# Kernel optimization log

Measured on AMD Instinct MI355X. Metric: run time of the kernel, lower is better.

## Reference

```python
import jax, jax.numpy as jnp
import numpy as np

N, F, E = 50000, 128, 800000
H, C1, C2 = 4, 32, 32  # heads, channel_in, channel_out
LRELU_SLOPE = 0.2
LN_EPS = 1e-5


def _gat_conv(x, src, dst, W_src, W_dst, att_src, att_dst, bias, n, h, c):
    # x: [n, f_in]; src/dst: [e] edge endpoints (message j->i)
    xs = (x @ W_src).reshape(n, h, c)  # source-side transform
    xd = (x @ W_dst).reshape(n, h, c)  # dest-side transform
    a_s = jnp.einsum('nhc,hc->nh', xs, att_src)  # [n,h]
    a_d = jnp.einsum('nhc,hc->nh', xd, att_dst)
    e = jax.nn.leaky_relu(a_s[src] + a_d[dst], LRELU_SLOPE)  # [E,h]
    m = jax.lax.stop_gradient(jax.ops.segment_max(e, dst, num_segments=n))
    ee = jnp.exp(e - m[dst])
    denom = jax.ops.segment_sum(ee, dst, num_segments=n)
    alpha = ee / (denom[dst] + 1e-16)  # segment softmax over incoming edges
    out = jax.ops.segment_sum(xs[src] * alpha[:, :, None], dst, num_segments=n)
    return out.reshape(n, h * c) + bias


def _layer_norm(x, gamma, beta):
    mu = jnp.mean(x, axis=-1, keepdims=True)
    var = jnp.var(x, axis=-1, keepdims=True)
    return (x - mu) * jax.lax.rsqrt(var + LN_EPS) * gamma + beta


def setup_inputs() -> dict:
    key = jax.random.key(0)
    ks = jax.random.split(key, 16)
    hid = H * C1  # 128
    out_dim = H * C2  # 128

    def glorot(k, shape, fan_in):
        return jax.random.normal(k, shape, dtype=jnp.float32) / np.sqrt(fan_in)

    x = jax.random.normal(ks[0], (N, F), dtype=jnp.float32)
    edge_index = jax.random.randint(ks[1], (2, E), 0, N, dtype=jnp.int32)

    return {
        'x': x,
        'edge_index': edge_index,
        # conv1 (in F -> H*C1)
        'W1_src': glorot(ks[2], (F, H * C1), F),
        'W1_dst': glorot(ks[3], (F, H * C1), F),
        'att1_src': glorot(ks[4], (H, C1), C1),
        'att1_dst': glorot(ks[5], (H, C1), C1),
        'b1': jnp.zeros((H * C1,), jnp.float32),
        # lin1 skip (F -> hid)
        'Wl1': glorot(ks[6], (F, hid), F),
        'bl1': jnp.zeros((hid,), jnp.float32),
        # LayerNorm over hid
        'gamma': jnp.ones((hid,), jnp.float32),
        'beta': jnp.zeros((hid,), jnp.float32),
        # conv2 (hid -> H*C2)
        'W2_src': glorot(ks[7], (hid, H * C2), hid),
        'W2_dst': glorot(ks[8], (hid, H * C2), hid),
        'att2_src': glorot(ks[9], (H, C2), C2),
        'att2_dst': glorot(ks[10], (H, C2), C2),
        'b2': jnp.zeros((H * C2,), jnp.float32),
        # lin2 skip (hid -> out_dim)
        'Wl2': glorot(ks[11], (hid, out_dim), hid),
        'bl2': jnp.zeros((out_dim,), jnp.float32),
    }


def reference(x, edge_index, W1_src, W1_dst, att1_src, att1_dst, b1, Wl1, bl1,
              gamma, beta, W2_src, W2_dst, att2_src, att2_dst, b2, Wl2, bl2):
    src, dst = edge_index[0], edge_index[1]
    h = _gat_conv(x, src, dst, W1_src, W1_dst, att1_src, att1_dst, b1, N, H, C1) \
        + (x @ Wl1 + bl1)
    h = jax.nn.relu(_layer_norm(h, gamma, beta))
    out = _gat_conv(h, src, dst, W2_src, W2_dst, att2_src, att2_dst, b2, N, H, C2) \
        + (h @ Wl2 + bl2)
    return out
```

## Files before the change

### kernel.cpp

```cpp
#include <hip/hip_runtime.h>

#define N_NODES 50000
#define E_EDGES 800000
#define LRELU 0.2f
#define LN_EPS 1e-5f
#define NBUCK 98
#define BSHIFT 9
#define BCAP 9216

typedef short bf16x8 __attribute__((ext_vector_type(8)));
typedef float f32x4 __attribute__((ext_vector_type(4)));

__device__ __forceinline__ ushort f2bf(float f) {
    uint u = __float_as_uint(f);
    u += 0x7FFF + ((u >> 16) & 1);
    return (ushort)(u >> 16);
}
__device__ __forceinline__ float bflo(uint u) { return __uint_as_float(u << 16); }
__device__ __forceinline__ float bfhi(uint u) { return __uint_as_float(u & 0xFFFF0000u); }

__global__ __launch_bounds__(256) void bucket_scatter_kernel(
    const int* __restrict__ src, const int* __restrict__ dst,
    int* __restrict__ bucketCursor, uint* __restrict__ pairs, int e)
{
    __shared__ int lhist[128];
    __shared__ int lscan[NBUCK];
    __shared__ int lcur[NBUCK];
    __shared__ int lbase[NBUCK];
    __shared__ uint stageW[2048];
    __shared__ int  stageA[2048];
    int t = threadIdx.x;
    int e0 = blockIdx.x * 2048;
    int count = min(2048, e - e0);

    if (t < 128) lhist[t] = 0;
    if (t < NBUCK) lcur[t] = 0;
    __syncthreads();

    int  bb[8];
    uint pk[8];
    #pragma unroll
    for (int q = 0; q < 8; ++q) {
        int li = t + q * 256;
        if (li < count) {
            int d = dst[e0 + li];
            int s = src[e0 + li];
            bb[q] = d >> BSHIFT;
            pk[q] = (uint)s | ((uint)(d & 511) << 16);
            atomicAdd(&lhist[bb[q]], 1);
        } else bb[q] = -1;
    }
    __syncthreads();

    int orig = (t < 128) ? lhist[t] : 0;
    #pragma unroll
    for (int off = 1; off < 128; off <<= 1) {
        int u = 0;
        if (t < 128 && t >= off) u = lhist[t - off];
        __syncthreads();
        if (t < 128) lhist[t] += u;
        __syncthreads();
    }
    if (t < NBUCK) {
        lscan[t] = lhist[t] - orig;
        lbase[t] = t * BCAP + (orig ? atomicAdd(&bucketCursor[t], orig) : 0);
    }
    __syncthreads();

    #pragma unroll
    for (int q = 0; q < 8; ++q) {
        if (bb[q] >= 0) {
            int slot = lscan[bb[q]] + atomicAdd(&lcur[bb[q]], 1);
            stageW[slot] = pk[q];
            stageA[slot] = lbase[bb[q]] + (slot - lscan[bb[q]]);
        }
    }
    __syncthreads();

    #pragma unroll
    for (int q = 0; q < 8; ++q) {
        int li = t + q * 256;
        if (li < count) pairs[stageA[li]] = stageW[li];
    }
}

__global__ __launch_bounds__(512) void bucket_sort_kernel(
    const uint* __restrict__ pairs, const int* __restrict__ bucketCursor,
    int* __restrict__ offs, ushort* __restrict__ degs,
    ushort* __restrict__ srcSorted, int n)
{
    __shared__ int cnt[512], cur[512], ls[512];
    int b = blockIdx.x, t = threadIdx.x;
    int base = b * BCAP;
    int m = bucketCursor[b];
    cnt[t] = 0; cur[t] = 0;
    __syncthreads();
    for (int i = t; i < m; i += 512)
        atomicAdd(&cnt[pairs[base + i] >> 16], 1);
    __syncthreads();
    int orig = cnt[t];
    ls[t] = orig;
    __syncthreads();
    #pragma unroll
    for (int off = 1; off < 512; off <<= 1) {
        int u = (t >= off) ? ls[t - off] : 0;
        __syncthreads();
        ls[t] += u;
        __syncthreads();
    }
    int excl = ls[t] - orig;
    int node = (b << BSHIFT) + t;
    if (node < n) {
        offs[node] = base + excl;
        degs[node] = (ushort)orig;
    }
    cnt[t] = excl;
    __syncthreads();
    for (int i = t; i < m; i += 512) {
        uint w = pairs[base + i];
        int dl = w >> 16;
        int pos = cnt[dl] + atomicAdd(&cur[dl], 1);
        srcSorted[base + pos] = (ushort)(w & 0xFFFFu);
    }
}

__global__ __launch_bounds__(256) void prep_all_kernel(
    const float* __restrict__ W1s, const float* __restrict__ Wl1,
    const float* __restrict__ W1d, const float* __restrict__ a1s,
    const float* __restrict__ a1d,
    const float* __restrict__ W2s, const float* __restrict__ Wl2,
    const float* __restrict__ W2d, const float* __restrict__ a2s,
    const float* __restrict__ a2d,
    ushort* __restrict__ Wt, ushort* __restrict__ Watt)
{
    int t = threadIdx.x;
    if (blockIdx.x < 256) {
        int idx = blockIdx.x * 256 + t;
        int lw = idx >> 14, rem = idx & 16383;
        int nn = rem >> 7, k = rem & 127;
        const float* W = (lw == 0) ? W1s : (lw == 1) ? Wl1 : (lw == 2) ? W2s : Wl2;
        Wt[idx] = f2bf(W[k * 128 + nn]);
    } else {
        int L = blockIdx.x - 256;
        const float* Ws = L ? W2s : W1s;
        const float* Wd = L ? W2d : W1d;
        const float* as = L ? a2s : a1s;
        const float* adv = L ? a2d : a1d;
        #pragma unroll
        for (int q = 0; q < 8; ++q) {
            int e = q * 256 + t;
            int c = e >> 7, f = e & 127;
            float v = 0.f;
            if (c < 8) {
                const float* W  = (c < 4) ? Ws : Wd;
                const float* av = (c < 4) ? as : adv;
                int h = c & 3;
                #pragma unroll
                for (int j = 0; j < 32; ++j)
                    v += W[f * 128 + h * 32 + j] * av[h * 32 + j];
            }
            Watt[L * 2048 + c * 128 + f] = f2bf(v);
        }
    }
}

template <int LAYER>
__global__ __launch_bounds__(256) void gemm_fused_kernel(
    const float* __restrict__ Afp, const ushort* __restrict__ Abf,
    const ushort* __restrict__ Wt, const ushort* __restrict__ Watt,
    ushort* __restrict__ Cbf, float* __restrict__ a_sd, int n)
{
    __shared__ ushort Asb[64][136];
    __shared__ ushort Wsb[128][136];
    __shared__ ushort Attb[16][136];
    const int z = blockIdx.x;
    const int row0 = blockIdx.y * 64;
    const int tid = threadIdx.x;

    if (LAYER == 0) {
        #pragma unroll
        for (int i = 0; i < 8; ++i) {
            int idx = tid + i * 256;
            int r = idx >> 5, c4 = idx & 31;
            int grow = row0 + r;
            float4 v = make_float4(0.f, 0.f, 0.f, 0.f);
            if (grow < n) v = *(const float4*)(Afp + (size_t)grow * 128 + c4 * 4);
            ushort4 o;
            o.x = f2bf(v.x); o.y = f2bf(v.y); o.z = f2bf(v.z); o.w = f2bf(v.w);
            *(ushort4*)&Asb[r][c4 * 4] = o;
        }
    } else {
        #pragma unroll
        for (int i = 0; i < 4; ++i) {
            int c = tid + i * 256;
            int r = c >> 4, o = c & 15;
            int grow = row0 + r;
            uint4 v = make_uint4(0, 0, 0, 0);
            if (grow < n) v = *(const uint4*)(Abf + (size_t)grow * 128 + o * 8);
            *(uint4*)&Asb[r][o * 8] = v;
        }
    }
    {
        const ushort* Wz = Wt + (size_t)(LAYER * 2 + z) * 16384;
        #pragma unroll
        for (int i = 0; i < 8; ++i) {
            int c = tid + i * 256;
            int r = c >> 4, o = c & 15;
            uint4 v = *(const uint4*)(Wz + r * 128 + o * 8);
            *(uint4*)&Wsb[r][o * 8] = v;
        }
    }
    if (z == 0) {
        int r = tid >> 4, o = tid & 15;
        uint4 v = *(const uint4*)(Watt + LAYER * 2048 + r * 128 + o * 8);
        *(uint4*)&Attb[r][o * 8] = v;
    }
    __syncthreads();

    const int w = tid >> 6, lane = tid & 63;
    const int wm = w >> 1, wn = w & 1;
    const int l15 = lane & 15, lg = lane >> 4;
    const bool doAtt = (z == 0) && (wn == 0);

    f32x4 acc[2][4];
    f32x4 accA[2];
    #pragma unroll
    for (int m = 0; m < 2; ++m) {
        accA[m] = (f32x4){0.f, 0.f, 0.f, 0.f};
        #pragma unroll
        for (int j = 0; j < 4; ++j)
            acc[m][j] = (f32x4){0.f, 0.f, 0.f, 0.f};
    }

    #pragma unroll
    for (int ks = 0; ks < 4; ++ks) {
        const int k0 = ks * 32 + 4 * lg;
        bf16x8 af[2], bfr[4];
        #pragma unroll
        for (int m = 0; m < 2; ++m) {
            const ushort* p = &Asb[wm * 32 + m * 16 + l15][k0];
            ushort4 lo = *(const ushort4*)p;
            ushort4 hi = *(const ushort4*)(p + 16);
            bf16x8 a;
            a[0] = (short)lo.x; a[1] = (short)lo.y; a[2] = (short)lo.z; a[3] = (short)lo.w;
            a[4] = (short)hi.x; a[5] = (short)hi.y; a[6] = (short)hi.z; a[7] = (short)hi.w;
            af[m] = a;
        }
        #pragma unroll
        for (int j = 0; j < 4; ++j) {
            const ushort* p = &Wsb[wn * 64 + j * 16 + l15][k0];
            ushort4 lo = *(const ushort4*)p;
            ushort4 hi = *(const ushort4*)(p + 16);
            bf16x8 b;
            b[0] = (short)lo.x; b[1] = (short)lo.y; b[2] = (short)lo.z; b[3] = (short)lo.w;
            b[4] = (short)hi.x; b[5] = (short)hi.y; b[6] = (short)hi.z; b[7] = (short)hi.w;
            bfr[j] = b;
        }
        #pragma unroll
        for (int m = 0; m < 2; ++m)
            #pragma unroll
            for (int j = 0; j < 4; ++j)
                acc[m][j] = __builtin_amdgcn_mfma_f32_16x16x32_bf16(
                    af[m], bfr[j], acc[m][j], 0, 0, 0);
        if (doAtt) {
            const ushort* p = &Attb[l15][k0];
            ushort4 lo = *(const ushort4*)p;
            ushort4 hi = *(const ushort4*)(p + 16);
            bf16x8 b;
            b[0] = (short)lo.x; b[1] = (short)lo.y; b[2] = (short)lo.z; b[3] = (short)lo.w;
            b[4] = (short)hi.x; b[5] = (short)hi.y; b[6] = (short)hi.z; b[7] = (short)hi.w;
            #pragma unroll
            for (int m = 0; m < 2; ++m)
                accA[m] = __builtin_amdgcn_mfma_f32_16x16x32_bf16(
                    af[m], b, accA[m], 0, 0, 0);
        }
    }

    if (doAtt && l15 < 8) {
        #pragma unroll
        for (int m = 0; m < 2; ++m)
            #pragma unroll
            for (int r = 0; r < 4; ++r) {
                int grow = row0 + wm * 32 + m * 16 + lg * 4 + r;
                if (grow < n) a_sd[(size_t)grow * 8 + l15] = accA[m][r];
            }
    }

    __syncthreads();
    ushort (*Cs)[136] = (ushort(*)[136])&Asb[0][0];
    #pragma unroll
    for (int m = 0; m < 2; ++m)
        #pragma unroll
        for (int j = 0; j < 4; ++j)
            #pragma unroll
            for (int r = 0; r < 4; ++r)
                Cs[wm * 32 + m * 16 + lg * 4 + r][wn * 64 + j * 16 + l15] =
                    f2bf(acc[m][j][r]);
    __syncthreads();
    #pragma unroll
    for (int i = 0; i < 4; ++i) {
        int u4 = tid + i * 256;
        int r = u4 >> 4, c8 = u4 & 15;
        int grow = row0 + r;
        if (grow < n) {
            uint4 v = *(const uint4*)&Cs[r][c8 * 8];
            *(uint4*)(Cbf + (size_t)grow * 256 + z * 128 + c8 * 8) = v;
        }
    }
}

template <int MODE>
__global__ __launch_bounds__(256) void aggregate_fused_kernel(
    const ushort* __restrict__ srcSorted, const int* __restrict__ offs,
    const ushort* __restrict__ degs,
    const ushort* __restrict__ bufbf,
    const float* __restrict__ a_sd,
    const float* __restrict__ bias_a, const float* __restrict__ bias_l,
    const float* __restrict__ gamma, const float* __restrict__ beta,
    ushort* __restrict__ hbf, float* __restrict__ out, int n)
{
    int node = (blockIdx.x * blockDim.x + threadIdx.x) >> 6;
    int lane = threadIdx.x & 63;
    if (node >= n) return;
    int beg = offs[node];
    int end = beg + degs[node];
    const int j = lane >> 4;
    const int g = lane & 15;
    const int h = g >> 2;
    const int he2 = (lane >> 3) & 3;

    float adh = 0.f;
    if (lane < 32) adh = a_sd[(size_t)node * 8 + 4 + he2];

    float acc[8] = {};
    float denp = 0.f;

    for (int t = beg; t < end; t += 8) {
        int s = 0; float ee = 0.f;
        if (lane < 32) {
            int idx = t + (lane & 7);
            int ic = (idx < end) ? idx : (end - 1);
            s = srcSorted[ic];
            float as = a_sd[(size_t)s * 8 + he2];
            float e = as + adh;
            e = (e > 0.f) ? e : LRELU * e;
            ee = (idx < end) ? __expf(e) : 0.f;
            denp += ee;
        }
        int   sA  = __shfl(s, j);
        int   sB  = __shfl(s, j + 4);
        float eeA = __shfl(ee, h * 8 + j);
        float eeB = __shfl(ee, h * 8 + j + 4);
        uint4 xA = *(const uint4*)(bufbf + (size_t)sA * 256 + g * 8);
        uint4 xB = *(const uint4*)(bufbf + (size_t)sB * 256 + g * 8);
        acc[0] = fmaf(eeA, bflo(xA.x), acc[0]);
        acc[1] = fmaf(eeA, bfhi(xA.x), acc[1]);
        acc[2] = fmaf(eeA, bflo(xA.y), acc[2]);
        acc[3] = fmaf(eeA, bfhi(xA.y), acc[3]);
        acc[4] = fmaf(eeA, bflo(xA.z), acc[4]);
        acc[5] = fmaf(eeA, bfhi(xA.z), acc[5]);
        acc[6] = fmaf(eeA, bflo(xA.w), acc[6]);
        acc[7] = fmaf(eeA, bfhi(xA.w), acc[7]);
        acc[0] = fmaf(eeB, bflo(xB.x), acc[0]);
        acc[1] = fmaf(eeB, bfhi(xB.x), acc[1]);
        acc[2] = fmaf(eeB, bflo(xB.y), acc[2]);
        acc[3] = fmaf(eeB, bfhi(xB.y), acc[3]);
        acc[4] = fmaf(eeB, bflo(xB.z), acc[4]);
        acc[5] = fmaf(eeB, bfhi(xB.z), acc[5]);
        acc[6] = fmaf(eeB, bflo(xB.w), acc[6]);
        acc[7] = fmaf(eeB, bfhi(xB.w), acc[7]);
    }

    #pragma unroll
    for (int c = 0; c < 8; ++c) {
        acc[c] += __shfl_xor(acc[c], 16);
        acc[c] += __shfl_xor(acc[c], 32);
    }
    denp += __shfl_xor(denp, 1);
    denp += __shfl_xor(denp, 2);
    denp += __shfl_xor(denp, 4);
    float den = __shfl(denp, (g >> 2) * 8);

    if (lane < 16) {
        float inv = 1.f / (den + 1e-16f);
        uint4 sk = *(const uint4*)(bufbf + (size_t)node * 256 + 128 + g * 8);
        float4 ba0 = *(const float4*)(bias_a + g * 8);
        float4 ba1 = *(const float4*)(bias_a + g * 8 + 4);
        float4 bl0 = *(const float4*)(bias_l + g * 8);
        float4 bl1 = *(const float4*)(bias_l + g * 8 + 4);
        float v[8];
        v[0] = acc[0] * inv + bflo(sk.x) + ba0.x + bl0.x;
        v[1] = acc[1] * inv + bfhi(sk.x) + ba0.y + bl0.y;
        v[2] = acc[2] * inv + bflo(sk.y) + ba0.z + bl0.z;
        v[3] = acc[3] * inv + bfhi(sk.y) + ba0.w + bl0.w;
        v[4] = acc[4] * inv + bflo(sk.z) + ba1.x + bl1.x;
        v[5] = acc[5] * inv + bfhi(sk.z) + ba1.y + bl1.y;
        v[6] = acc[6] * inv + bflo(sk.w) + ba1.z + bl1.z;
        v[7] = acc[7] * inv + bfhi(sk.w) + ba1.w + bl1.w;

        if (MODE == 0) {
            float sum = 0.f, sq = 0.f;
            #pragma unroll
            for (int c = 0; c < 8; ++c) { sum += v[c]; sq += v[c] * v[c]; }
            #pragma unroll
            for (int off = 1; off < 16; off <<= 1) {
                sum += __shfl_xor(sum, off);
                sq  += __shfl_xor(sq, off);
            }
            float mu = sum * (1.f / 128.f);
            float var = sq * (1.f / 128.f) - mu * mu;
            float rs = rsqrtf(var + LN_EPS);
            float4 gm0 = *(const float4*)(gamma + g * 8);
            float4 gm1 = *(const float4*)(gamma + g * 8 + 4);
            float4 bt0 = *(const float4*)(beta + g * 8);
            float4 bt1 = *(const float4*)(beta + g * 8 + 4);
            float o[8];
            o[0] = fmaxf((v[0] - mu) * rs * gm0.x + bt0.x, 0.f);
            o[1] = fmaxf((v[1] - mu) * rs * gm0.y + bt0.y, 0.f);
            o[2] = fmaxf((v[2] - mu) * rs * gm0.z + bt0.z, 0.f);
            o[3] = fmaxf((v[3] - mu) * rs * gm0.w + bt0.w, 0.f);
            o[4] = fmaxf((v[4] - mu) * rs * gm1.x + bt1.x, 0.f);
            o[5] = fmaxf((v[5] - mu) * rs * gm1.y + bt1.y, 0.f);
            o[6] = fmaxf((v[6] - mu) * rs * gm1.z + bt1.z, 0.f);
            o[7] = fmaxf((v[7] - mu) * rs * gm1.w + bt1.w, 0.f);
            uint4 st;
            st.x = (uint)f2bf(o[0]) | ((uint)f2bf(o[1]) << 16);
            st.y = (uint)f2bf(o[2]) | ((uint)f2bf(o[3]) << 16);
            st.z = (uint)f2bf(o[4]) | ((uint)f2bf(o[5]) << 16);
            st.w = (uint)f2bf(o[6]) | ((uint)f2bf(o[7]) << 16);
            *(uint4*)(hbf + (size_t)node * 128 + g * 8) = st;
        } else {
            *(float4*)(out + (size_t)node * 128 + g * 8) =
                make_float4(v[0], v[1], v[2], v[3]);
            *(float4*)(out + (size_t)node * 128 + g * 8 + 4) =
                make_float4(v[4], v[5], v[6], v[7]);
        }
    }
}

extern "C" void kernel_launch(void* const* d_in, const int* in_sizes, int n_in,
                              void* d_out, int out_size, void* d_ws, size_t ws_size,
                              hipStream_t stream) {
    const float* x       = (const float*)d_in[0];
    const int*   ei      = (const int*)d_in[1];
    const int*   src     = ei;
    const int*   dst     = ei + E_EDGES;
    const float* W1_src  = (const float*)d_in[2];
    const float* W1_dst  = (const float*)d_in[3];
    const float* att1_s  = (const float*)d_in[4];
    const float* att1_d  = (const float*)d_in[5];
    const float* b1      = (const float*)d_in[6];
    const float* Wl1     = (const float*)d_in[7];
    const float* bl1     = (const float*)d_in[8];
    const float* gamma   = (const float*)d_in[9];
    const float* beta    = (const float*)d_in[10];
    const float* W2_src  = (const float*)d_in[11];
    const float* W2_dst  = (const float*)d_in[12];
    const float* att2_s  = (const float*)d_in[13];
    const float* att2_d  = (const float*)d_in[14];
    const float* b2      = (const float*)d_in[15];
    const float* Wl2     = (const float*)d_in[16];
    const float* bl2     = (const float*)d_in[17];
    float* out = (float*)d_out;

    char* p = (char*)d_ws;
    float* a_sd        = (float*)p;      p += (size_t)N_NODES * 8 * 4;
    int* offs          = (int*)p;        p += (size_t)N_NODES * 4;
    int* bucketCursor  = (int*)p;        p += 128 * 4;
    uint* pairs        = (uint*)p;       p += (size_t)NBUCK * BCAP * 4;
    ushort* degs       = (ushort*)p;     p += (size_t)N_NODES * 2;
    ushort* hbf        = (ushort*)p;     p += (size_t)N_NODES * 128 * 2;
    ushort* bufbf      = (ushort*)p;     p += (size_t)N_NODES * 256 * 2;
    ushort* Wt         = (ushort*)p;     p += (size_t)4 * 16384 * 2;
    ushort* Watt       = (ushort*)p;     p += (size_t)2 * 2048 * 2;
    ushort* srcSorted  = (ushort*)p;     p += (size_t)NBUCK * BCAP * 2;

    dim3 ggrid(2, (N_NODES + 63) / 64);
    int edge_blocks = (E_EDGES + 2047) / 2048;
    int wave_grid   = (N_NODES + 3) / 4;

    hipMemsetAsync(bucketCursor, 0, NBUCK * sizeof(int), stream);
    bucket_scatter_kernel<<<edge_blocks, 256, 0, stream>>>(src, dst, bucketCursor, pairs, E_EDGES);
    bucket_sort_kernel<<<NBUCK, 512, 0, stream>>>(pairs, bucketCursor, offs, degs, srcSorted, N_NODES);

    prep_all_kernel<<<258, 256, 0, stream>>>(
        W1_src, Wl1, W1_dst, att1_s, att1_d,
        W2_src, Wl2, W2_dst, att2_s, att2_d, Wt, Watt);

    gemm_fused_kernel<0><<<ggrid, 256, 0, stream>>>(x, nullptr, Wt, Watt, bufbf, a_sd, N_NODES);
    aggregate_fused_kernel<0><<<wave_grid, 256, 0, stream>>>(
        srcSorted, offs, degs, bufbf, a_sd, b1, bl1, gamma, beta, hbf, nullptr, N_NODES);

    gemm_fused_kernel<1><<<ggrid, 256, 0, stream>>>(nullptr, hbf, Wt, Watt, bufbf, a_sd, N_NODES);
    aggregate_fused_kernel<1><<<wave_grid, 256, 0, stream>>>(
        srcSorted, offs, degs, bufbf, a_sd, b2, bl2, nullptr, nullptr, nullptr, out, N_NODES);
}
```

Before: 293.4 us.

## Use finer dst buckets, fold cursor reset into prep, widen aggregation edge batch

Edges are now bucketed by 256-node destination ranges (196 buckets), so the sort runs with 256-thread blocks across twice as many blocks. The scatter kernel handles 4096 edges per block. The bucket-cursor memset is replaced by an extra block in the weight-prep kernel, which now runs first, saving one launch. The aggregation kernel has all 64 lanes compute attention logits and processes 16 edges per iteration with four gathered rows in flight instead of two, raising memory-level parallelism but wasting more work on low-degree tails.

```diff
diff --git a/kernel.cpp b/kernel.cpp
--- a/kernel.cpp
+++ b/kernel.cpp
@@ -4,9 +4,9 @@
 #define E_EDGES 800000
 #define LRELU 0.2f
 #define LN_EPS 1e-5f
-#define NBUCK 98
-#define BSHIFT 9
-#define BCAP 9216
+#define NBUCK 196
+#define BSHIFT 8
+#define BCAP 4608
 
 typedef short bf16x8 __attribute__((ext_vector_type(8)));
 typedef float f32x4 __attribute__((ext_vector_type(4)));
@@ -23,42 +23,41 @@
     const int* __restrict__ src, const int* __restrict__ dst,
     int* __restrict__ bucketCursor, uint* __restrict__ pairs, int e)
 {
-    __shared__ int lhist[128];
+    __shared__ int lhist[256];
     __shared__ int lscan[NBUCK];
     __shared__ int lcur[NBUCK];
     __shared__ int lbase[NBUCK];
-    __shared__ uint stageW[2048];
-    __shared__ int  stageA[2048];
+    __shared__ uint stageW[4096];
+    __shared__ int  stageA[4096];
     int t = threadIdx.x;
-    int e0 = blockIdx.x * 2048;
-    int count = min(2048, e - e0);
-
-    if (t < 128) lhist[t] = 0;
+    int e0 = blockIdx.x * 4096;
+    int count = min(4096, e - e0);
+
+    lhist[t] = 0;
     if (t < NBUCK) lcur[t] = 0;
     __syncthreads();
 
-    int  bb[8];
-    uint pk[8];
-    #pragma unroll
-    for (int q = 0; q < 8; ++q) {
+    int  bb[16];
+    uint pk[16];
+    #pragma unroll
+    for (int q = 0; q < 16; ++q) {
         int li = t + q * 256;
         if (li < count) {
             int d = dst[e0 + li];
             int s = src[e0 + li];
             bb[q] = d >> BSHIFT;
-            pk[q] = (uint)s | ((uint)(d & 511) << 16);
+            pk[q] = (uint)s | ((uint)(d & 255) << 16);
             atomicAdd(&lhist[bb[q]], 1);
         } else bb[q] = -1;
     }
     __syncthreads();
 
-    int orig = (t < 128) ? lhist[t] : 0;
-    #pragma unroll
-    for (int off = 1; off < 128; off <<= 1) {
-        int u = 0;
-        if (t < 128 && t >= off) u = lhist[t - off];
+    int orig = lhist[t];
+    #pragma unroll
+    for (int off = 1; off < 256; off <<= 1) {
+        int u = (t >= off) ? lhist[t - off] : 0;
         __syncthreads();
-        if (t < 128) lhist[t] += u;
+        lhist[t] += u;
         __syncthreads();
     }
     if (t < NBUCK) {
@@ -68,7 +67,7 @@
     __syncthreads();
 
     #pragma unroll
-    for (int q = 0; q < 8; ++q) {
+    for (int q = 0; q < 16; ++q) {
         if (bb[q] >= 0) {
             int slot = lscan[bb[q]] + atomicAdd(&lcur[bb[q]], 1);
             stageW[slot] = pk[q];
@@ -78,31 +77,31 @@
     __syncthreads();
 
     #pragma unroll
-    for (int q = 0; q < 8; ++q) {
+    for (int q = 0; q < 16; ++q) {
         int li = t + q * 256;
         if (li < count) pairs[stageA[li]] = stageW[li];
     }
 }
 
-__global__ __launch_bounds__(512) void bucket_sort_kernel(
+__global__ __launch_bounds__(256) void bucket_sort_kernel(
     const uint* __restrict__ pairs, const int* __restrict__ bucketCursor,
     int* __restrict__ offs, ushort* __restrict__ degs,
     ushort* __restrict__ srcSorted, int n)
 {
-    __shared__ int cnt[512], cur[512], ls[512];
+    __shared__ int cnt[256], cur[256], ls[256];
     int b = blockIdx.x, t = threadIdx.x;
     int base = b * BCAP;
     int m = bucketCursor[b];
     cnt[t] = 0; cur[t] = 0;
     __syncthreads();
-    for (int i = t; i < m; i += 512)
+    for (int i = t; i < m; i += 256)
         atomicAdd(&cnt[pairs[base + i] >> 16], 1);
     __syncthreads();
     int orig = cnt[t];
     ls[t] = orig;
     __syncthreads();
     #pragma unroll
-    for (int off = 1; off < 512; off <<= 1) {
+    for (int off = 1; off < 256; off <<= 1) {
         int u = (t >= off) ? ls[t - off] : 0;
         __syncthreads();
         ls[t] += u;
@@ -116,7 +115,7 @@
     }
     cnt[t] = excl;
     __syncthreads();
-    for (int i = t; i < m; i += 512) {
+    for (int i = t; i < m; i += 256) {
         uint w = pairs[base + i];
         int dl = w >> 16;
         int pos = cnt[dl] + atomicAdd(&cur[dl], 1);
@@ -131,7 +130,8 @@
     const float* __restrict__ W2s, const float* __restrict__ Wl2,
     const float* __restrict__ W2d, const float* __restrict__ a2s,
     const float* __restrict__ a2d,
-    ushort* __restrict__ Wt, ushort* __restrict__ Watt)
+    ushort* __restrict__ Wt, ushort* __restrict__ Watt,
+    int* __restrict__ bucketCursor)
 {
     int t = threadIdx.x;
     if (blockIdx.x < 256) {
@@ -140,7 +140,7 @@
         int nn = rem >> 7, k = rem & 127;
         const float* W = (lw == 0) ? W1s : (lw == 1) ? Wl1 : (lw == 2) ? W2s : Wl2;
         Wt[idx] = f2bf(W[k * 128 + nn]);
-    } else {
+    } else if (blockIdx.x < 258) {
         int L = blockIdx.x - 256;
         const float* Ws = L ? W2s : W1s;
         const float* Wd = L ? W2d : W1d;
@@ -161,6 +161,8 @@
             }
             Watt[L * 2048 + c * 128 + f] = f2bf(v);
         }
+    } else {
+        if (t < NBUCK) bucketCursor[t] = 0;
     }
 }
 
@@ -324,35 +326,39 @@
     if (node >= n) return;
     int beg = offs[node];
     int end = beg + degs[node];
-    const int j = lane >> 4;
-    const int g = lane & 15;
-    const int h = g >> 2;
-    const int he2 = (lane >> 3) & 3;
-
-    float adh = 0.f;
-    if (lane < 32) adh = a_sd[(size_t)node * 8 + 4 + he2];
+    const int q  = lane & 15;
+    const int hh = lane >> 4;
+    const int g  = lane & 15;
+    const int j  = lane >> 4;
+    const int h  = g >> 2;
+
+    float adh = a_sd[(size_t)node * 8 + 4 + hh];
 
     float acc[8] = {};
     float denp = 0.f;
 
-    for (int t = beg; t < end; t += 8) {
-        int s = 0; float ee = 0.f;
-        if (lane < 32) {
-            int idx = t + (lane & 7);
-            int ic = (idx < end) ? idx : (end - 1);
-            s = srcSorted[ic];
-            float as = a_sd[(size_t)s * 8 + he2];
-            float e = as + adh;
-            e = (e > 0.f) ? e : LRELU * e;
-            ee = (idx < end) ? __expf(e) : 0.f;
-            denp += ee;
-        }
+    for (int t = beg; t < end; t += 16) {
+        int idx = t + q;
+        int ic = (idx < end) ? idx : (end - 1);
+        int s = srcSorted[ic];
+        float as = a_sd[(size_t)s * 8 + hh];
+        float e = as + adh;
+        e = (e > 0.f) ? e : LRELU * e;
+        float ee = (idx < end) ? __expf(e) : 0.f;
+        denp += ee;
+
         int   sA  = __shfl(s, j);
         int   sB  = __shfl(s, j + 4);
-        float eeA = __shfl(ee, h * 8 + j);
-        float eeB = __shfl(ee, h * 8 + j + 4);
+        int   sC  = __shfl(s, j + 8);
+        int   sD  = __shfl(s, j + 12);
+        float eeA = __shfl(ee, h * 16 + j);
+        float eeB = __shfl(ee, h * 16 + j + 4);
+        float eeC = __shfl(ee, h * 16 + j + 8);
+        float eeD = __shfl(ee, h * 16 + j + 12);
         uint4 xA = *(const uint4*)(bufbf + (size_t)sA * 256 + g * 8);
         uint4 xB = *(const uint4*)(bufbf + (size_t)sB * 256 + g * 8);
+        uint4 xC = *(const uint4*)(bufbf + (size_t)sC * 256 + g * 8);
+        uint4 xD = *(const uint4*)(bufbf + (size_t)sD * 256 + g * 8);
         acc[0] = fmaf(eeA, bflo(xA.x), acc[0]);
         acc[1] = fmaf(eeA, bfhi(xA.x), acc[1]);
         acc[2] = fmaf(eeA, bflo(xA.y), acc[2]);
@@ -369,6 +375,22 @@
         acc[5] = fmaf(eeB, bfhi(xB.z), acc[5]);
         acc[6] = fmaf(eeB, bflo(xB.w), acc[6]);
         acc[7] = fmaf(eeB, bfhi(xB.w), acc[7]);
+        acc[0] = fmaf(eeC, bflo(xC.x), acc[0]);
+        acc[1] = fmaf(eeC, bfhi(xC.x), acc[1]);
+        acc[2] = fmaf(eeC, bflo(xC.y), acc[2]);
+        acc[3] = fmaf(eeC, bfhi(xC.y), acc[3]);
+        acc[4] = fmaf(eeC, bflo(xC.z), acc[4]);
+        acc[5] = fmaf(eeC, bfhi(xC.z), acc[5]);
+        acc[6] = fmaf(eeC, bflo(xC.w), acc[6]);
+        acc[7] = fmaf(eeC, bfhi(xC.w), acc[7]);
+        acc[0] = fmaf(eeD, bflo(xD.x), acc[0]);
+        acc[1] = fmaf(eeD, bfhi(xD.x), acc[1]);
+        acc[2] = fmaf(eeD, bflo(xD.y), acc[2]);
+        acc[3] = fmaf(eeD, bfhi(xD.y), acc[3]);
+        acc[4] = fmaf(eeD, bflo(xD.z), acc[4]);
+        acc[5] = fmaf(eeD, bfhi(xD.z), acc[5]);
+        acc[6] = fmaf(eeD, bflo(xD.w), acc[6]);
+        acc[7] = fmaf(eeD, bfhi(xD.w), acc[7]);
     }
 
     #pragma unroll
@@ -379,7 +401,8 @@
     denp += __shfl_xor(denp, 1);
     denp += __shfl_xor(denp, 2);
     denp += __shfl_xor(denp, 4);
-    float den = __shfl(denp, (g >> 2) * 8);
+    denp += __shfl_xor(denp, 8);
+    float den = __shfl(denp, h * 16);
 
     if (lane < 16) {
         float inv = 1.f / (den + 1e-16f);
@@ -466,7 +489,7 @@
     char* p = (char*)d_ws;
     float* a_sd        = (float*)p;      p += (size_t)N_NODES * 8 * 4;
     int* offs          = (int*)p;        p += (size_t)N_NODES * 4;
-    int* bucketCursor  = (int*)p;        p += 128 * 4;
+    int* bucketCursor  = (int*)p;        p += 256 * 4;
     uint* pairs        = (uint*)p;       p += (size_t)NBUCK * BCAP * 4;
     ushort* degs       = (ushort*)p;     p += (size_t)N_NODES * 2;
     ushort* hbf        = (ushort*)p;     p += (size_t)N_NODES * 128 * 2;
@@ -476,16 +499,14 @@
     ushort* srcSorted  = (ushort*)p;     p += (size_t)NBUCK * BCAP * 2;
 
     dim3 ggrid(2, (N_NODES + 63) / 64);
-    int edge_blocks = (E_EDGES + 2047) / 2048;
+    int edge_blocks = (E_EDGES + 4095) / 4096;
     int wave_grid   = (N_NODES + 3) / 4;
 
-    hipMemsetAsync(bucketCursor, 0, NBUCK * sizeof(int), stream);
+    prep_all_kernel<<<259, 256, 0, stream>>>(
+        W1_src, Wl1, W1_dst, att1_s, att1_d,
+        W2_src, Wl2, W2_dst, att2_s, att2_d, Wt, Watt, bucketCursor);
     bucket_scatter_kernel<<<edge_blocks, 256, 0, stream>>>(src, dst, bucketCursor, pairs, E_EDGES);
-    bucket_sort_kernel<<<NBUCK, 512, 0, stream>>>(pairs, bucketCursor, offs, degs, srcSorted, N_NODES);
-
-    prep_all_kernel<<<258, 256, 0, stream>>>(
-        W1_src, Wl1, W1_dst, att1_s, att1_d,
-        W2_src, Wl2, W2_dst, att2_s, att2_d, Wt, Watt);
+    bucket_sort_kernel<<<NBUCK, 256, 0, stream>>>(pairs, bucketCursor, offs, degs, srcSorted, N_NODES);
 
     gemm_fused_kernel<0><<<ggrid, 256, 0, stream>>>(x, nullptr, Wt, Watt, bufbf, a_sd, N_NODES);
     aggregate_fused_kernel<0><<<wave_grid, 256, 0, stream>>>(
```

Result: no change. 287.7 us (-2.0%).
